# Optimization experiments

Hardware: AMD Instinct MI355X
Metric: run time of the kernel (lower is better)

Reference implementation:

```python
import jax, jax.numpy as jnp
import numpy as np

B, S, E = 2, 2048, 2048
NQ, NKV, HD = 16, 4, 128
WINDOW = 512
ROPE_BASE = 10000.0


def _rope(x):
    # x: [B, H, S, HD], interleaved even/odd rotation
    half = HD // 2
    freqs = 1.0 / (ROPE_BASE ** (2.0 * jnp.arange(half, dtype=jnp.float32) / HD))
    pos = jnp.arange(x.shape[2], dtype=jnp.float32)
    ang = pos[:, None] * freqs[None, :]            # [S, HD/2]
    cos = jnp.cos(ang)[None, None].astype(x.dtype)  # [1,1,S,HD/2]
    sin = jnp.sin(ang)[None, None].astype(x.dtype)
    xe = x[..., 0::2]
    xo = x[..., 1::2]
    re = xe * cos - xo * sin
    ro = xe * sin + xo * cos
    return jnp.stack([re, ro], axis=-1).reshape(x.shape)


def setup_inputs() -> dict:
    key = jax.random.key(0)
    ks = jax.random.split(key, 9)
    s_in = 1.0 / np.sqrt(E)
    s_out = 1.0 / np.sqrt(NQ * HD)
    return {
        "x": jax.random.normal(ks[0], (B, S, E), jnp.float32),
        "Wq": jax.random.normal(ks[1], (E, NQ * HD), jnp.float32) * s_in,
        "bq": jax.random.normal(ks[2], (NQ * HD,), jnp.float32) * 0.01,
        "Wk": jax.random.normal(ks[3], (E, NKV * HD), jnp.float32) * s_in,
        "bk": jax.random.normal(ks[4], (NKV * HD,), jnp.float32) * 0.01,
        "Wv": jax.random.normal(ks[5], (E, NKV * HD), jnp.float32) * s_in,
        "bv": jax.random.normal(ks[6], (NKV * HD,), jnp.float32) * 0.01,
        "Wo": jax.random.normal(ks[7], (NQ * HD, E), jnp.float32) * s_out,
        "bo": jax.random.normal(ks[8], (E,), jnp.float32) * 0.01,
    }


def reference(x, Wq, bq, Wk, bk, Wv, bv, Wo, bo):
    b, s, _ = x.shape
    q = (x @ Wq + bq).reshape(b, s, NQ, HD).transpose(0, 2, 1, 3)   # [B,NQ,S,HD]
    k = (x @ Wk + bk).reshape(b, s, NKV, HD).transpose(0, 2, 1, 3)  # [B,NKV,S,HD]
    v = (x @ Wv + bv).reshape(b, s, NKV, HD).transpose(0, 2, 1, 3)
    q = _rope(q)
    k = _rope(k)
    rep = NQ // NKV
    k = jnp.repeat(k, rep, axis=1)  # [B,NQ,S,HD], matches torch repeat pattern
    v = jnp.repeat(v, rep, axis=1)
    scores = jnp.einsum("bhqd,bhkd->bhqk", q, k) / np.sqrt(HD)
    i = jnp.arange(s)[:, None]
    j = jnp.arange(s)[None, :]
    allowed = (j <= i) & ((i - j) <= WINDOW)  # sliding-window causal mask
    scores = jnp.where(allowed[None, None], scores, -jnp.inf)
    weights = jax.nn.softmax(scores, axis=-1)
    out = jnp.einsum("bhqk,bhkd->bhqd", weights, v)
    out = out.transpose(0, 2, 1, 3).reshape(b, s, NQ * HD)
    return out @ Wo + bo
```

## Files before the change

kernel.cpp:

```cpp
#include <hip/hip_runtime.h>
#include <hip/hip_bf16.h>
#include <math.h>

#define BB 2
#define SS 2048
#define EE 2048
#define NQ 16
#define NKV 4
#define HD 128
#define WINDOW 512

typedef __hip_bfloat16 bf16;
typedef short short8 __attribute__((ext_vector_type(8)));
typedef float f32x4 __attribute__((ext_vector_type(4)));

__device__ __forceinline__ float toF(bf16 v) { return __bfloat162float(v); }
__device__ __forceinline__ bf16 toB(float v) { return __float2bfloat16(v); }

__device__ __forceinline__ void gld_lds16(const void* g, void* l) {
    __builtin_amdgcn_global_load_lds(
        (const __attribute__((address_space(1))) void*)g,
        (__attribute__((address_space(3))) void*)l, 16, 0, 0);
}

template <int V> __device__ __forceinline__ void waitvm() {
    if constexpr (V == 8)      asm volatile("s_waitcnt vmcnt(8)" ::: "memory");
    else if constexpr (V == 6) asm volatile("s_waitcnt vmcnt(6)" ::: "memory");
    else if constexpr (V == 4) asm volatile("s_waitcnt vmcnt(4)" ::: "memory");
    else if constexpr (V == 3) asm volatile("s_waitcnt vmcnt(3)" ::: "memory");
    else                       asm volatile("s_waitcnt vmcnt(0)" ::: "memory");
}

__global__ __launch_bounds__(256) void convert_bf16(const float* __restrict__ in,
                                                    bf16* __restrict__ out, int n) {
    int i = (blockIdx.x * 256 + threadIdx.x) * 4;
    if (i >= n) return;
    const float4 v = *(const float4*)(in + i);
    bf16 o[4] = {toB(v.x), toB(v.y), toB(v.z), toB(v.w)};
    *(uint2*)(out + i) = *(const uint2*)o;
}

__global__ __launch_bounds__(256) void convert_transpose(const float* __restrict__ in,
                                                         bf16* __restrict__ out,
                                                         int K, int N) {
    __shared__ float tile[32][33];
    const int t = threadIdx.x;
    const int tx = t & 31, ty = t >> 5;
    const int n0 = blockIdx.x * 32, k0 = blockIdx.y * 32;
#pragma unroll
    for (int r = 0; r < 4; r++)
        tile[ty + r * 8][tx] = in[(size_t)(k0 + ty + r * 8) * N + n0 + tx];
    __syncthreads();
#pragma unroll
    for (int r = 0; r < 4; r++)
        out[(size_t)(n0 + ty + r * 8) * K + k0 + tx] = toB(tile[tx][ty + r * 8]);
}

__global__ __launch_bounds__(256) void convert_transpose_qkv(
    const float* __restrict__ Wq, const float* __restrict__ Wk,
    const float* __restrict__ Wv, bf16* __restrict__ out) {
    __shared__ float tile[32][33];
    const int t = threadIdx.x;
    const int tx = t & 31, ty = t >> 5;
    const int n0 = blockIdx.x * 32, k0 = blockIdx.y * 32;
    const float* src; int N, nl0;
    if (n0 < 2048)      { src = Wq; N = 2048; nl0 = n0; }
    else if (n0 < 2560) { src = Wk; N = 512;  nl0 = n0 - 2048; }
    else                { src = Wv; N = 512;  nl0 = n0 - 2560; }
#pragma unroll
    for (int r = 0; r < 4; r++)
        tile[ty + r * 8][tx] = src[(size_t)(k0 + ty + r * 8) * N + nl0 + tx];
    __syncthreads();
#pragma unroll
    for (int r = 0; r < 4; r++)
        out[(size_t)(n0 + ty + r * 8) * 2048 + k0 + tx] = toB(tile[tx][ty + r * 8]);
}

template <int MODE, int BM, int BN, int WARPS_M>
__global__ __launch_bounds__(512, 2) void mfma_gemm_v3(
    const bf16* __restrict__ A, const bf16* __restrict__ BT,
    const float* __restrict__ b0, const float* __restrict__ b1,
    const float* __restrict__ b2,
    float* __restrict__ Yf,
    bf16* __restrict__ Yq, bf16* __restrict__ Yk, bf16* __restrict__ Yv,
    int M, int N, int K) {
    constexpr int WARPS_N = 8 / WARPS_M;
    constexpr int NI = BM / WARPS_M / 16;
    constexpr int NJ = BN / WARPS_N / 16;
    constexpr int LA = BM / 128;
    constexpr int LB = BN / 128;
    constexpr int PL = LA + LB;

    __shared__ __align__(16) bf16 As[2][2][BM * 32];
    __shared__ __align__(16) bf16 Bs[2][2][BN * 32];

    const int t = threadIdx.x;
    const int lane = t & 63;
    const int w = t >> 6;
    const int wm = w / WARPS_N;
    const int wn = w % WARPS_N;
    const int m0 = blockIdx.y * BM, n0 = blockIdx.x * BN;
    const int lr = lane & 15;
    const int lq = lane >> 4;
    const int NT = K >> 6;

    auto stA = [&](int bi, int kk, int kt) {
#pragma unroll
        for (int l = 0; l < LA; l++) {
            const int c = w * LA + l;
            gld_lds16(A + (size_t)(m0 + c * 16 + (lane >> 2)) * K +
                          kt * 64 + kk * 32 + (lane & 3) * 8,
                      &As[bi][kk][c * 512]);
        }
    };
    auto stB = [&](int bi, int kk, int kt) {
#pragma unroll
        for (int l = 0; l < LB; l++) {
            const int c = w * LB + l;
            gld_lds16(BT + (size_t)(n0 + c * 16 + (lane >> 2)) * K +
                           kt * 64 + kk * 32 + (lane & 3) * 8,
                      &Bs[bi][kk][c * 512]);
        }
    };

    f32x4 acc[NI][NJ];
#pragma unroll
    for (int i = 0; i < NI; i++)
#pragma unroll
        for (int j = 0; j < NJ; j++) acc[i][j] = (f32x4)0.f;

    auto phase = [&](int bi, int kk) {
        const bf16* Aslc = &As[bi][kk][0];
        const bf16* Bslc = &Bs[bi][kk][0];
        short8 af[NI], bfv[NJ];
#pragma unroll
        for (int i = 0; i < NI; i++)
            af[i] = *(const short8*)(Aslc + (wm * (NI * 16) + i * 16 + lr) * 32 + lq * 8);
#pragma unroll
        for (int j = 0; j < NJ; j++)
            bfv[j] = *(const short8*)(Bslc + (wn * (NJ * 16) + j * 16 + lr) * 32 + lq * 8);
        __builtin_amdgcn_s_setprio(1);
#pragma unroll
        for (int i = 0; i < NI; i++)
#pragma unroll
            for (int j = 0; j < NJ; j++)
                acc[i][j] = __builtin_amdgcn_mfma_f32_16x16x32_bf16(af[i], bfv[j],
                                                                    acc[i][j], 0, 0, 0);
        __builtin_amdgcn_s_setprio(0);
    };

    stA(0, 0, 0); stB(0, 0, 0);
    stA(0, 1, 0); stB(0, 1, 0);

    for (int kt = 0; kt < NT; kt++) {
        const int bi = kt & 1;
        const bool pf = (kt + 1 < NT);
        if (pf) { stA(bi ^ 1, 0, kt + 1); stB(bi ^ 1, 0, kt + 1); waitvm<2 * PL>(); }
        else    { waitvm<PL>(); }
        __builtin_amdgcn_s_barrier();
        __builtin_amdgcn_sched_barrier(0);
        phase(bi, 0);
        if (pf) { stA(bi ^ 1, 1, kt + 1); stB(bi ^ 1, 1, kt + 1); waitvm<2 * PL>(); }
        else    { waitvm<0>(); }
        __builtin_amdgcn_s_barrier();
        __builtin_amdgcn_sched_barrier(0);
        phase(bi, 1);
        __builtin_amdgcn_s_barrier();
    }

    if (MODE == 0) {
#pragma unroll
        for (int j = 0; j < NJ; j++) {
            const int col = n0 + wn * (NJ * 16) + j * 16 + lr;
            const float bj = b0[col];
#pragma unroll
            for (int i = 0; i < NI; i++) {
                const int row = m0 + wm * (NI * 16) + i * 16 + lq * 4;
#pragma unroll
                for (int r = 0; r < 4; r++)
                    Yf[(size_t)(row + r) * N + col] = acc[i][j][r] + bj;
            }
        }
    } else if (n0 < 2560) {
        bf16* outp; const float* bias; int ldc, c0;
        if (n0 < 2048) { outp = Yq; bias = b0; ldc = 2048; c0 = n0; }
        else           { outp = Yk; bias = b1; ldc = 512;  c0 = n0 - 2048; }
#pragma unroll
        for (int j = 0; j < NJ; j++) {
            const int col = c0 + wn * (NJ * 16) + j * 16 + lr;
            const float bj = bias[col];
            const int d2 = (col & 127) >> 1;
            const bool odd = col & 1;
            const float freq = __expf(-0.14384103622589045f * (float)d2);
#pragma unroll
            for (int i = 0; i < NI; i++) {
                const int row = m0 + wm * (NI * 16) + i * 16 + lq * 4;
#pragma unroll
                for (int r = 0; r < 4; r++) {
                    const float v = acc[i][j][r] + bj;
                    const float p = __shfl_xor(v, 1, 64);
                    const float ang = (float)((row + r) & (SS - 1)) * freq;
                    float sn, cs;
                    __sincosf(ang, &sn, &cs);
                    const float o = odd ? (p * sn + v * cs) : (v * cs - p * sn);
                    outp[(size_t)(row + r) * ldc + col] = toB(o);
                }
            }
        }
    } else {
        const int c0 = n0 - 2560;
#pragma unroll
        for (int j = 0; j < NJ; j++) {
            const int col = c0 + wn * (NJ * 16) + j * 16 + lr;
            const float bj = b2[col];
            const int hkv = col >> 7, d = col & 127;
#pragma unroll
            for (int i = 0; i < NI; i++) {
                const int row = m0 + wm * (NI * 16) + i * 16 + lq * 4;
                const int bb = row >> 11, sr = row & (SS - 1);
                union { bf16 b[4]; uint2 u; } o4;
#pragma unroll
                for (int r = 0; r < 4; r++) o4.b[r] = toB(acc[i][j][r] + bj);
                *(uint2*)(Yv + (((size_t)bb * NKV + hkv) * HD + d) * SS + sr) = o4.u;
            }
        }
    }
}

__global__ __launch_bounds__(256) void attn_mfma(const bf16* __restrict__ Q,
                                                 const bf16* __restrict__ K,
                                                 const bf16* __restrict__ VT,
                                                 bf16* __restrict__ Oout) {
    __shared__ bf16 Ks[64 * 128];
    __shared__ bf16 Vs[128 * 64];
    __shared__ bf16 Ps[4 * 16 * 72];

    const int t = threadIdx.x;
    const int lane = t & 63;
    const int w = t >> 6;
    const int q0 = blockIdx.x * 64;
    const int h = blockIdx.y;
    const int b = blockIdx.z;
    const int hkv = h >> 2;
    const int lr = lane & 15;
    const int lq = lane >> 4;
    const float scale = 0.08838834764831845f;

    short8 aq[4];
    {
        const int q = q0 + w * 16 + lr;
        const bf16* qp = Q + (((size_t)b * SS + q) * NQ + h) * HD + lq * 8;
#pragma unroll
        for (int ks = 0; ks < 4; ks++) aq[ks] = *(const short8*)(qp + ks * 32);
    }

    const int krow = w * 16 + (lane >> 4);
    const int vrow = w * 32 + (lane >> 3);
    const bf16* Kbase = K + ((size_t)b * SS * NKV + hkv) * HD;
    const bf16* Vbase = VT + (((size_t)b * NKV + hkv) * HD) * SS;

    f32x4 Oa[8];
#pragma unroll
    for (int nb = 0; nb < 8; nb++) Oa[nb] = (f32x4)0.f;
    float mprev[4] = {-3.0e38f, -3.0e38f, -3.0e38f, -3.0e38f};
    float lsum[4] = {0.f, 0.f, 0.f, 0.f};

    bf16* Pw = Ps + w * 16 * 72;
    const int jstart = (q0 >= WINDOW) ? (q0 - WINDOW) : 0;

    for (int c0 = jstart; c0 <= q0; c0 += 64) {
        __syncthreads();
#pragma unroll
        for (int s = 0; s < 4; s++) {
            const int r_ = krow + s * 4;
            const int g_ = (lane & 15) ^ (r_ & 7);
            gld_lds16(Kbase + (size_t)(c0 + r_) * (NKV * HD) + g_ * 8,
                      Ks + (w * 16 + s * 4) * 128);
        }
#pragma unroll
        for (int s = 0; s < 4; s++) {
            const int d_ = vrow + s * 8;
            const int g_ = (lane & 7) ^ (d_ & 7);
            gld_lds16(Vbase + (size_t)d_ * SS + c0 + g_ * 8,
                      Vs + (w * 32 + s * 8) * 64);
        }
        __syncthreads();

        f32x4 sa[4];
#pragma unroll
        for (int nb = 0; nb < 4; nb++) sa[nb] = (f32x4)0.f;
#pragma unroll
        for (int ks = 0; ks < 4; ks++) {
#pragma unroll
            for (int nb = 0; nb < 4; nb++) {
                const int slot = (ks * 4 + lq) ^ (lr & 7);
                short8 bk = *(const short8*)(Ks + (nb * 16 + lr) * 128 + slot * 8);
                sa[nb] = __builtin_amdgcn_mfma_f32_16x16x32_bf16(aq[ks], bk, sa[nb], 0, 0, 0);
            }
        }

        const int rowb = q0 + w * 16 + lq * 4;
        const bool noMask = (c0 + 63 <= q0 + w * 16) &&
                            (q0 + w * 16 + 15 - c0 <= WINDOW);
        float pr[4][4], alpha[4];
#pragma unroll
        for (int r = 0; r < 4; r++) {
            const int row = rowb + r;
            float sv[4];
            float mx = -3.0e38f;
            if (noMask) {
#pragma unroll
                for (int nb = 0; nb < 4; nb++) {
                    const float s = sa[nb][r] * scale;
                    sv[nb] = s;
                    mx = fmaxf(mx, s);
                }
            } else {
#pragma unroll
                for (int nb = 0; nb < 4; nb++) {
                    const int col = c0 + nb * 16 + lr;
                    const bool valid = (col <= row) && (row - col <= WINDOW);
                    const float s = valid ? sa[nb][r] * scale : -3.0e38f;
                    sv[nb] = s;
                    mx = fmaxf(mx, s);
                }
            }
#pragma unroll
            for (int off = 1; off < 16; off <<= 1) mx = fmaxf(mx, __shfl_xor(mx, off, 64));
            const float mn = fmaxf(fmaxf(mprev[r], mx), -1.0e30f);
            alpha[r] = __expf(mprev[r] - mn);
            mprev[r] = mn;
            float rs = 0.f;
#pragma unroll
            for (int nb = 0; nb < 4; nb++) {
                const float p = __expf(sv[nb] - mn);
                pr[r][nb] = p;
                rs += p;
            }
#pragma unroll
            for (int off = 1; off < 16; off <<= 1) rs += __shfl_xor(rs, off, 64);
            lsum[r] = lsum[r] * alpha[r] + rs;
        }

#pragma unroll
        for (int r = 0; r < 4; r++)
#pragma unroll
            for (int nb = 0; nb < 4; nb++)
                Pw[(lq * 4 + r) * 72 + nb * 16 + lr] = toB(pr[r][nb]);

#pragma unroll
        for (int nb = 0; nb < 8; nb++)
#pragma unroll
            for (int r = 0; r < 4; r++) Oa[nb][r] *= alpha[r];
#pragma unroll
        for (int ks = 0; ks < 2; ks++) {
            short8 pa = *(const short8*)(Pw + lr * 72 + ks * 32 + lq * 8);
#pragma unroll
            for (int nb = 0; nb < 8; nb++) {
                const int slot = (ks * 4 + lq) ^ (lr & 7);
                short8 bv = *(const short8*)(Vs + (nb * 16 + lr) * 64 + slot * 8);
                Oa[nb] = __builtin_amdgcn_mfma_f32_16x16x32_bf16(pa, bv, Oa[nb], 0, 0, 0);
            }
        }
    }

    float linv[4];
#pragma unroll
    for (int r = 0; r < 4; r++) linv[r] = 1.f / lsum[r];
    const int rowb = q0 + w * 16 + lq * 4;
#pragma unroll
    for (int nb = 0; nb < 8; nb++)
#pragma unroll
        for (int r = 0; r < 4; r++)
            Oout[(((size_t)b * SS + rowb + r) * NQ + h) * HD + nb * 16 + lr] =
                toB(Oa[nb][r] * linv[r]);
}

extern "C" void kernel_launch(void* const* d_in, const int* in_sizes, int n_in,
                              void* d_out, int out_size, void* d_ws, size_t ws_size,
                              hipStream_t stream) {
    const float* x  = (const float*)d_in[0];
    const float* Wq = (const float*)d_in[1];
    const float* bq = (const float*)d_in[2];
    const float* Wk = (const float*)d_in[3];
    const float* bk = (const float*)d_in[4];
    const float* Wv = (const float*)d_in[5];
    const float* bv = (const float*)d_in[6];
    const float* Wo = (const float*)d_in[7];
    const float* bo = (const float*)d_in[8];
    float* out = (float*)d_out;

    const int M   = BB * SS;
    const int DQ  = NQ * HD;
    const int DKV = NKV * HD;
    const int NPK = DQ + 2 * DKV;

    bf16* xb     = (bf16*)d_ws;
    bf16* WqkvT  = xb + (size_t)M * EE;
    bf16* WoT    = WqkvT + (size_t)NPK * EE;
    bf16* Qb     = WoT + (size_t)EE * DQ;
    bf16* Kb     = Qb + (size_t)M * DQ;
    bf16* Vb     = Kb + (size_t)M * DKV;

    convert_bf16<<<(M * EE / 4 + 255) / 256, 256, 0, stream>>>(x, xb, M * EE);
    convert_transpose_qkv<<<dim3(NPK / 32, EE / 32), 256, 0, stream>>>(Wq, Wk, Wv, WqkvT);
    convert_transpose<<<dim3(DQ / 32, DQ / 32), 256, 0, stream>>>(Wo, WoT, DQ, EE);

    mfma_gemm_v3<1, 256, 256, 2><<<dim3(NPK / 256, M / 256), 512, 0, stream>>>(
        xb, WqkvT, bq, bk, bv, nullptr, Qb, Kb, Vb, M, NPK, EE);

    attn_mfma<<<dim3(SS / 64, NQ, BB), 256, 0, stream>>>(Qb, Kb, Vb, Qb);

    mfma_gemm_v3<0, 256, 128, 4><<<dim3(EE / 128, M / 256), 512, 0, stream>>>(
        Qb, WoT, bo, nullptr, nullptr, out, nullptr, nullptr, nullptr, M, EE, DQ);
}
```

Measured before the change: 327.5 us.

## Rewrite GEMM with 4-stage LDS ring, register double-buffered fragments, swizzle, new tiles

Replaces the double-buffered GEMM with a 4-slot LDS ring that prefetches three k-steps of 32 ahead. MFMA fragments are double-buffered in registers, so LDS reads for the next step overlap the current step's MFMAs. An XOR swizzle is added to the LDS layout to reduce bank conflicts, and warps are fixed at 2x4. Tile shapes change (128x384 for QKV, 128x256 for the output projection), which moves Q/K/V output boundaries to per-column handling in the epilogue. The cost is more LDS and fragment registers, which could limit occupancy.

```diff
diff --git a/kernel.cpp b/kernel.cpp
--- a/kernel.cpp
+++ b/kernel.cpp
@@ -76,96 +76,105 @@
         out[(size_t)(n0 + ty + r * 8) * 2048 + k0 + tx] = toB(tile[tx][ty + r * 8]);
 }
 
-template <int MODE, int BM, int BN, int WARPS_M>
-__global__ __launch_bounds__(512, 2) void mfma_gemm_v3(
+template <int MODE, int BM, int BN>
+__global__ __launch_bounds__(512, 2) void mfma_gemm_v4(
     const bf16* __restrict__ A, const bf16* __restrict__ BT,
     const float* __restrict__ b0, const float* __restrict__ b1,
     const float* __restrict__ b2,
     float* __restrict__ Yf,
     bf16* __restrict__ Yq, bf16* __restrict__ Yk, bf16* __restrict__ Yv,
     int M, int N, int K) {
-    constexpr int WARPS_N = 8 / WARPS_M;
-    constexpr int NI = BM / WARPS_M / 16;
-    constexpr int NJ = BN / WARPS_N / 16;
+    constexpr int NI = BM / 32;
+    constexpr int NJ = BN / 64;
     constexpr int LA = BM / 128;
     constexpr int LB = BN / 128;
-    constexpr int PL = LA + LB;
-
-    __shared__ __align__(16) bf16 As[2][2][BM * 32];
-    __shared__ __align__(16) bf16 Bs[2][2][BN * 32];
+    constexpr int SL = LA + LB;
+
+    __shared__ __align__(16) bf16 As[4][BM * 32];
+    __shared__ __align__(16) bf16 Bs[4][BN * 32];
 
     const int t = threadIdx.x;
     const int lane = t & 63;
     const int w = t >> 6;
-    const int wm = w / WARPS_N;
-    const int wn = w % WARPS_N;
+    const int wm = w >> 2;
+    const int wn = w & 3;
     const int m0 = blockIdx.y * BM, n0 = blockIdx.x * BN;
     const int lr = lane & 15;
     const int lq = lane >> 4;
-    const int NT = K >> 6;
-
-    auto stA = [&](int bi, int kk, int kt) {
+    const int NT = K >> 5;
+
+    auto stage = [&](int s) {
+        bf16* Ad = &As[s & 3][0];
 #pragma unroll
         for (int l = 0; l < LA; l++) {
             const int c = w * LA + l;
-            gld_lds16(A + (size_t)(m0 + c * 16 + (lane >> 2)) * K +
-                          kt * 64 + kk * 32 + (lane & 3) * 8,
-                      &As[bi][kk][c * 512]);
-        }
-    };
-    auto stB = [&](int bi, int kk, int kt) {
+            const int row = c * 16 + (lane >> 2);
+            const int g = (lane & 3) ^ ((row >> 1) & 3);
+            gld_lds16(A + (size_t)(m0 + row) * K + s * 32 + g * 8, Ad + c * 512);
+        }
+        bf16* Bd = &Bs[s & 3][0];
 #pragma unroll
         for (int l = 0; l < LB; l++) {
             const int c = w * LB + l;
-            gld_lds16(BT + (size_t)(n0 + c * 16 + (lane >> 2)) * K +
-                           kt * 64 + kk * 32 + (lane & 3) * 8,
-                      &Bs[bi][kk][c * 512]);
+            const int row = c * 16 + (lane >> 2);
+            const int g = (lane & 3) ^ ((row >> 1) & 3);
+            gld_lds16(BT + (size_t)(n0 + row) * K + s * 32 + g * 8, Bd + c * 512);
         }
     };
 
+    auto loadfr = [&](int s, short8 (&fA)[NI], short8 (&fB)[NJ]) {
+        const bf16* Asl = &As[s & 3][0];
+        const bf16* Bsl = &Bs[s & 3][0];
+#pragma unroll
+        for (int i = 0; i < NI; i++) {
+            const int row = wm * (NI * 16) + i * 16 + lr;
+            const int sl = lq ^ ((row >> 1) & 3);
+            fA[i] = *(const short8*)(Asl + row * 32 + sl * 8);
+        }
+#pragma unroll
+        for (int j = 0; j < NJ; j++) {
+            const int row = wn * (NJ * 16) + j * 16 + lr;
+            const int sl = lq ^ ((row >> 1) & 3);
+            fB[j] = *(const short8*)(Bsl + row * 32 + sl * 8);
+        }
+    };
+
     f32x4 acc[NI][NJ];
 #pragma unroll
     for (int i = 0; i < NI; i++)
 #pragma unroll
         for (int j = 0; j < NJ; j++) acc[i][j] = (f32x4)0.f;
 
-    auto phase = [&](int bi, int kk) {
-        const bf16* Aslc = &As[bi][kk][0];
-        const bf16* Bslc = &Bs[bi][kk][0];
-        short8 af[NI], bfv[NJ];
+    auto region = [&](int r, short8 (&fAc)[NI], short8 (&fBc)[NJ],
+                             short8 (&fAn)[NI], short8 (&fBn)[NJ]) {
+        if (r + 3 < NT) stage(r + 3);
+        if (r + 1 < NT) loadfr(r + 1, fAn, fBn);
+        __builtin_amdgcn_sched_barrier(0);
+        __builtin_amdgcn_s_setprio(1);
 #pragma unroll
         for (int i = 0; i < NI; i++)
-            af[i] = *(const short8*)(Aslc + (wm * (NI * 16) + i * 16 + lr) * 32 + lq * 8);
-#pragma unroll
-        for (int j = 0; j < NJ; j++)
-            bfv[j] = *(const short8*)(Bslc + (wn * (NJ * 16) + j * 16 + lr) * 32 + lq * 8);
-        __builtin_amdgcn_s_setprio(1);
-#pragma unroll
-        for (int i = 0; i < NI; i++)
 #pragma unroll
             for (int j = 0; j < NJ; j++)
-                acc[i][j] = __builtin_amdgcn_mfma_f32_16x16x32_bf16(af[i], bfv[j],
+                acc[i][j] = __builtin_amdgcn_mfma_f32_16x16x32_bf16(fAc[i], fBc[j],
                                                                     acc[i][j], 0, 0, 0);
         __builtin_amdgcn_s_setprio(0);
+        asm volatile("s_waitcnt lgkmcnt(0)" ::: "memory");
+        if (r + 3 < NT) waitvm<SL>(); else waitvm<0>();
+        __builtin_amdgcn_sched_barrier(0);
+        __builtin_amdgcn_s_barrier();
     };
 
-    stA(0, 0, 0); stB(0, 0, 0);
-    stA(0, 1, 0); stB(0, 1, 0);
-
-    for (int kt = 0; kt < NT; kt++) {
-        const int bi = kt & 1;
-        const bool pf = (kt + 1 < NT);
-        if (pf) { stA(bi ^ 1, 0, kt + 1); stB(bi ^ 1, 0, kt + 1); waitvm<2 * PL>(); }
-        else    { waitvm<PL>(); }
-        __builtin_amdgcn_s_barrier();
-        __builtin_amdgcn_sched_barrier(0);
-        phase(bi, 0);
-        if (pf) { stA(bi ^ 1, 1, kt + 1); stB(bi ^ 1, 1, kt + 1); waitvm<2 * PL>(); }
-        else    { waitvm<0>(); }
-        __builtin_amdgcn_s_barrier();
-        __builtin_amdgcn_sched_barrier(0);
-        phase(bi, 1);
-        __builtin_amdgcn_s_barrier();
+    stage(0); stage(1); stage(2);
+    waitvm<SL>();
+    __builtin_amdgcn_s_barrier();
+    short8 fA0[NI], fB0[NJ], fA1[NI], fB1[NJ];
+    loadfr(0, fA0, fB0);
+    asm volatile("s_waitcnt lgkmcnt(0)" ::: "memory");
+    __builtin_amdgcn_sched_barrier(0);
+
+    for (int r = 0; r < NT; r += 2) {
+        region(r,     fA0, fB0, fA1, fB1);
+        region(r + 1, fA1, fB1, fA0, fB0);
     }
 
     if (MODE == 0) {
@@ -181,47 +190,45 @@
                     Yf[(size_t)(row + r) * N + col] = acc[i][j][r] + bj;
             }
         }
-    } else if (n0 < 2560) {
-        bf16* outp; const float* bias; int ldc, c0;
-        if (n0 < 2048) { outp = Yq; bias = b0; ldc = 2048; c0 = n0; }
-        else           { outp = Yk; bias = b1; ldc = 512;  c0 = n0 - 2048; }
+    } else {
 #pragma unroll
         for (int j = 0; j < NJ; j++) {
-            const int col = c0 + wn * (NJ * 16) + j * 16 + lr;
-            const float bj = bias[col];
-            const int d2 = (col & 127) >> 1;
-            const bool odd = col & 1;
-            const float freq = __expf(-0.14384103622589045f * (float)d2);
-#pragma unroll
-            for (int i = 0; i < NI; i++) {
-                const int row = m0 + wm * (NI * 16) + i * 16 + lq * 4;
-#pragma unroll
-                for (int r = 0; r < 4; r++) {
-                    const float v = acc[i][j][r] + bj;
-                    const float p = __shfl_xor(v, 1, 64);
-                    const float ang = (float)((row + r) & (SS - 1)) * freq;
-                    float sn, cs;
-                    __sincosf(ang, &sn, &cs);
-                    const float o = odd ? (p * sn + v * cs) : (v * cs - p * sn);
-                    outp[(size_t)(row + r) * ldc + col] = toB(o);
+            const int gcol = n0 + wn * (NJ * 16) + j * 16 + lr;
+            if (gcol < 2560) {
+                bf16* outp; const float* bias; int ldc, col;
+                if (gcol < 2048) { outp = Yq; bias = b0; ldc = 2048; col = gcol; }
+                else             { outp = Yk; bias = b1; ldc = 512;  col = gcol - 2048; }
+                const float bj = bias[col];
+                const int d2 = (col & 127) >> 1;
+                const bool odd = col & 1;
+                const float freq = __expf(-0.14384103622589045f * (float)d2);
+#pragma unroll
+                for (int i = 0; i < NI; i++) {
+                    const int row = m0 + wm * (NI * 16) + i * 16 + lq * 4;
+#pragma unroll
+                    for (int r = 0; r < 4; r++) {
+                        const float v = acc[i][j][r] + bj;
+                        const float p = __shfl_xor(v, 1, 64);
+                        const float ang = (float)((row + r) & (SS - 1)) * freq;
+                        float sn, cs;
+                        __sincosf(ang, &sn, &cs);
+                        const float o = odd ? (p * sn + v * cs) : (v * cs - p * sn);
+                        outp[(size_t)(row + r) * ldc + col] = toB(o);
+                    }
                 }
-            }
-        }
-    } else {
-        const int c0 = n0 - 2560;
-#pragma unroll
-        for (int j = 0; j < NJ; j++) {
-            const int col = c0 + wn * (NJ * 16) + j * 16 + lr;
-            const float bj = b2[col];
-            const int hkv = col >> 7, d = col & 127;
-#pragma unroll
-            for (int i = 0; i < NI; i++) {
-                const int row = m0 + wm * (NI * 16) + i * 16 + lq * 4;
-                const int bb = row >> 11, sr = row & (SS - 1);
-                union { bf16 b[4]; uint2 u; } o4;
-#pragma unroll
-                for (int r = 0; r < 4; r++) o4.b[r] = toB(acc[i][j][r] + bj);
-                *(uint2*)(Yv + (((size_t)bb * NKV + hkv) * HD + d) * SS + sr) = o4.u;
+            } else {
+                const int col = gcol - 2560;
+                const float bj = b2[col];
+                const int hkv = col >> 7, d = col & 127;
+#pragma unroll
+                for (int i = 0; i < NI; i++) {
+                    const int row = m0 + wm * (NI * 16) + i * 16 + lq * 4;
+                    const int bb = row >> 11, sr = row & (SS - 1);
+                    union { bf16 b[4]; uint2 u; } o4;
+#pragma unroll
+                    for (int r = 0; r < 4; r++) o4.b[r] = toB(acc[i][j][r] + bj);
+                    *(uint2*)(Yv + (((size_t)bb * NKV + hkv) * HD + d) * SS + sr) = o4.u;
+                }
             }
         }
     }
@@ -406,11 +413,11 @@
     convert_transpose_qkv<<<dim3(NPK / 32, EE / 32), 256, 0, stream>>>(Wq, Wk, Wv, WqkvT);
     convert_transpose<<<dim3(DQ / 32, DQ / 32), 256, 0, stream>>>(Wo, WoT, DQ, EE);
 
-    mfma_gemm_v3<1, 256, 256, 2><<<dim3(NPK / 256, M / 256), 512, 0, stream>>>(
+    mfma_gemm_v4<1, 128, 384><<<dim3(NPK / 384, M / 128), 512, 0, stream>>>(
         xb, WqkvT, bq, bk, bv, nullptr, Qb, Kb, Vb, M, NPK, EE);
 
     attn_mfma<<<dim3(SS / 64, NQ, BB), 256, 0, stream>>>(Qb, Kb, Vb, Qb);
 
-    mfma_gemm_v3<0, 256, 128, 4><<<dim3(EE / 128, M / 256), 512, 0, stream>>>(
+    mfma_gemm_v4<0, 128, 256><<<dim3(EE / 256, M / 128), 512, 0, stream>>>(
         Qb, WoT, bo, nullptr, nullptr, out, nullptr, nullptr, nullptr, M, EE, DQ);
 }
```

After: 332.8 us. Within noise of the previous version (+1.6%).
